# Kernel tuning notes

Measured on AMD Instinct MI355X. Metric: run time of the kernel, lower is better.

Reference implementation:

```python
import jax, jax.numpy as jnp
import numpy as np

B = 512      # streamlines (graphs in the batch)
L = 128      # points per streamline
M = L - 1    # edges per direction per streamline == conv output length
IN = 3       # 3-D coordinates
K = 5        # kNN neighbors (self included, as in PyG knn)
FOV = 5      # conv kernel; odd so conv out length == M, matching the batch vector
PAD = FOV // 2
NC = 2
EPS = 1e-5


def _bn(x, g, b, m, v):
    # inference-mode BatchNorm1d
    return (x - m) * jax.lax.rsqrt(v + EPS) * g + b


def setup_inputs():
    key = jax.random.key(0)
    ks = jax.random.split(key, 20)
    r = lambda i, shape: jax.random.normal(ks[i], shape, jnp.float32) * 0.05
    ones = lambda n: jnp.ones((n,), jnp.float32)
    zeros = lambda n: jnp.zeros((n,), jnp.float32)
    pos = jax.random.normal(ks[0], (B * L, IN), jnp.float32)
    # consecutive-point (forward) edges, streamline-major order
    base = (jnp.arange(B)[:, None] * L + jnp.arange(M)[None, :]).reshape(-1)
    fwd = jnp.stack([base, base + 1]).astype(jnp.int32)          # [2, B*M]
    eidx = jnp.concatenate([fwd, fwd], axis=1)                   # [2, 2*B*M]; first half overwritten in forward
    batch = jnp.repeat(jnp.arange(B, dtype=jnp.int32), L)        # per-point graph id
    lengths = jnp.full((B,), L, dtype=jnp.int32)
    return dict(
        pos=pos, eidx=eidx, batch=batch, lengths=lengths,
        conv1_w=r(1, (FOV, 2 * IN, 64)), conv1_b=r(2, (64,)),
        bn1_g=ones(64), bn1_b=zeros(64), bn1_m=r(3, (64,)), bn1_v=ones(64),
        edge_w=r(4, (2 * 64, 128)), edge_b=r(5, (128,)),
        bn2_g=ones(128), bn2_b=zeros(128), bn2_m=r(6, (128,)), bn2_v=ones(128),
        lin1_w=r(7, (64 + 128, 1024)), lin1_b=r(8, (1024,)),
        bn3_g=ones(1024), bn3_b=zeros(1024), bn3_m=r(9, (1024,)), bn3_v=ones(1024),
        m1_w=r(10, (1024, 512)), m1_b=r(11, (512,)),
        bn4_g=ones(512), bn4_b=zeros(512), bn4_m=r(12, (512,)), bn4_v=ones(512),
        m2_w=r(13, (512, 256)), m2_b=r(14, (256,)),
        bn5_g=ones(256), bn5_b=zeros(256), bn5_m=r(15, (256,)), bn5_v=ones(256),
        out_w=r(16, (256, NC)), out_b=r(17, (NC,)),
    )


def reference(pos, eidx, batch, lengths,
              conv1_w, conv1_b, bn1_g, bn1_b, bn1_m, bn1_v,
              edge_w, edge_b, bn2_g, bn2_b, bn2_m, bn2_v,
              lin1_w, lin1_b, bn3_g, bn3_b, bn3_m, bn3_v,
              m1_w, m1_b, bn4_g, bn4_b, bn4_m, bn4_v,
              m2_w, m2_b, bn5_g, bn5_b, bn5_m, bn5_v,
              out_w, out_b):
    E = eidx.shape[1]
    half = eidx[:, E // 2:]
    # eidx[:, :E//2] = eidx[:, E//2:].flip(1)
    eidx = jnp.concatenate([half[:, ::-1], half], axis=1)
    # irregular gather: edge features [E, 2*IN]
    feats = jnp.concatenate([pos[eidx[1]] - pos[eidx[0]], pos[eidx[0]]], axis=1)
    x = feats.reshape(2 * B, M, 2 * IN)                            # folded direction+batch
    # Conv1d (cross-correlation) -> BN -> ReLU, channels-last layout
    x = jax.lax.conv_general_dilated(x, conv1_w, (1,), [(PAD, PAD)],
                                     dimension_numbers=('NWC', 'WIO', 'NWC')) + conv1_b
    x = jax.nn.relu(_bn(x, bn1_g, bn1_b, bn1_m, bn1_v))            # [2B, M, 64]
    # direction symmetrization: max(first half, second half flipped on batch & length)
    x = jnp.maximum(x[:B], x[B:][::-1, ::-1, :])                   # [B, M, 64]
    x1 = x.reshape(B * M, 64)
    # ---- DynamicEdgeConv: per-streamline kNN graph + edge MLP + max aggregation ----
    xg = x1.reshape(B, M, 64)
    sq = jnp.sum(xg * xg, axis=-1)                                 # [B, M]
    dist = sq[:, :, None] + sq[:, None, :] - 2.0 * jnp.einsum('bmd,bnd->bmn', xg, xg)
    _, idx = jax.lax.top_k(-dist, K)                               # [B, M, K] (self included)
    xj = jax.vmap(lambda xs, ix: xs[ix])(xg, idx)                  # [B, M, K, 64]
    xi = jnp.broadcast_to(xg[:, :, None, :], xj.shape)
    ef = jnp.concatenate([xi, xj - xi], axis=-1)                   # [B, M, K, 128]
    ef = _bn(jax.nn.relu(ef @ edge_w + edge_b), bn2_g, bn2_b, bn2_m, bn2_v)
    x2 = jnp.max(ef, axis=2).reshape(B * M, 128)                   # max aggr over neighbors
    # ---- lin1 + global max pool + classifier MLP (dropout = identity in eval) ----
    h = jnp.concatenate([x1, x2], axis=1)                          # [N, 192]
    h = _bn(jax.nn.relu(h @ lin1_w + lin1_b), bn3_g, bn3_b, bn3_m, bn3_v)  # [N, 1024]
    g = jnp.max(h.reshape(B, M, 1024), axis=1)                     # global_max_pool -> [B, 1024]
    g = _bn(jax.nn.relu(g @ m1_w + m1_b), bn4_g, bn4_b, bn4_m, bn4_v)
    g = _bn(jax.nn.relu(g @ m2_w + m2_b), bn5_g, bn5_b, bn5_m, bn5_v)
    return g @ out_w + out_b                                       # [B, NC]
```

## Files before the change

kernel.cpp:

```cpp
#include <hip/hip_runtime.h>

#define BB 512
#define LL 128
#define MM 127
#define EPS 1e-5f

typedef _Float16 half4 __attribute__((ext_vector_type(4)));
typedef _Float16 half8 __attribute__((ext_vector_type(8)));
typedef float f32x16 __attribute__((ext_vector_type(16)));

#define HB_PITCH 384
#define HB_BATCH 49152

__global__ __launch_bounds__(256) void k0_prep(
    const float* __restrict__ lw, char* __restrict__ lwT,
    const float* __restrict__ ew, char* __restrict__ ewT,
    const float* __restrict__ m1w, char* __restrict__ m1wT,
    const float* __restrict__ m2w, char* __restrict__ m2wT)
{
  int tid = threadIdx.x;
  __shared__ float ws2[256][32];
  if (blockIdx.x < 32) {
    int c0 = blockIdx.x * 32;
    __shared__ float wcol[192][32];
    for (int i = tid; i < 192 * 32; i += 256) {
      int k = i >> 5, c = i & 31;
      wcol[k][c] = lw[k * 1024 + c0 + c];
    }
    __syncthreads();
    for (int j = tid; j < 768; j += 256) {
      int kg = j >> 5, c = j & 31;
      half8 v;
#pragma unroll
      for (int jj = 0; jj < 8; jj++) v[jj] = (_Float16)wcol[kg * 8 + jj][c];
      int cc = c0 + c;
      *(half8*)(lwT + cc * HB_PITCH + ((kg * 16) ^ ((cc & 7) << 4))) = v;
    }
  } else if (blockIdx.x == 32) {
    __shared__ float es[128][128];
    for (int i = tid; i < 128 * 128; i += 256) es[i >> 7][i & 127] = ew[i];
    __syncthreads();
    for (int i = tid; i < 256 * 8; i += 256) {
      int c = i >> 3, kg = i & 7;
      half8 v;
#pragma unroll
      for (int jj = 0; jj < 8; jj++) {
        int k = kg * 8 + jj;
        float val = (c < 128) ? (es[k][c] - es[64 + k][c]) : es[64 + k][c - 128];
        v[jj] = (_Float16)val;
      }
      *(half8*)(ewT + c * 128 + ((kg * 16) ^ ((c & 7) << 4))) = v;
    }
  } else {
    const float* src; char* dst; int N, K, c0, k0;
    if (blockIdx.x < 97) {
      int bb = blockIdx.x - 33;
      src = m1w; dst = m1wT; N = 512; K = 1024;
      c0 = (bb >> 2) * 32; k0 = (bb & 3) * 256;
    } else {
      int bb = blockIdx.x - 97;
      src = m2w; dst = m2wT; N = 256; K = 512;
      c0 = (bb >> 1) * 32; k0 = (bb & 1) * 256;
    }
    for (int i = tid; i < 256 * 32; i += 256) {
      int k = i >> 5, c = i & 31;
      ws2[k][c] = src[(size_t)(k0 + k) * N + c0 + c];
    }
    __syncthreads();
    for (int j = tid; j < 32 * 32; j += 256) {
      int kg = j >> 5, c = j & 31;
      half8 v;
#pragma unroll
      for (int jj = 0; jj < 8; jj++) v[jj] = (_Float16)ws2[kg * 8 + jj][c];
      int cc = c0 + c;
      *(half8*)(dst + (size_t)cc * (2 * K) + ((2 * (k0 + kg * 8)) ^ ((cc & 7) << 4))) = v;
    }
  }
}

__global__ __launch_bounds__(256) void k1a_conv(
    const float* __restrict__ pos, const float* __restrict__ cw,
    const float* __restrict__ cb, const float* __restrict__ g1,
    const float* __restrict__ b1, const float* __restrict__ m1,
    const float* __restrict__ v1, char* __restrict__ hb,
    float* __restrict__ xgr)
{
  int b = blockIdx.x;
  int tid = threadIdx.x;
  __shared__ float fpad[132][8];

  if (tid < 40) {
    int rr = tid >> 3;
    int row = (rr < 2) ? rr : (127 + rr);
    fpad[row][tid & 7] = 0.f;
  }
  const float* pb = pos + b * LL * 3;
  for (int i = tid; i < MM * 6; i += 256) {
    int m = i / 6, c = i % 6;
    float v = (c < 3) ? (pb[(m + 1) * 3 + c] - pb[m * 3 + c]) : pb[m * 3 + c - 3];
    fpad[m + 2][c] = v;
  }
  int orow = BB - 1 - b;
  char* hbb = hb + (size_t)orow * HB_BATCH;
  float* xgb = xgr + (size_t)orow * 8192;
  if (tid < 8) *(float4*)(hbb + 127 * HB_PITCH + tid * 16) = make_float4(0.f, 0.f, 0.f, 0.f);
  if (tid < 16) *(float4*)(xgb + 127 * 64 + tid * 4) = make_float4(0.f, 0.f, 0.f, 0.f);

  int c = tid & 63, cg = tid >> 6;
  float wreg[30];
#pragma unroll
  for (int t = 0; t < 5; t++)
#pragma unroll
    for (int ci = 0; ci < 6; ci++) wreg[t * 6 + ci] = cw[(t * 6 + ci) * 64 + c];
  float s1 = g1[c] * rsqrtf(v1[c] + EPS);
  float t1 = (cb[c] - m1[c]) * s1 + b1[c];
  __syncthreads();

#pragma unroll
  for (int it = 0; it < 8; it++) {
    int chunk = cg + 4 * it;
    int m0 = chunk * 4;
    float4 fa[8], fb[8];
#pragma unroll
    for (int r = 0; r < 8; r++) {
      fa[r] = *(const float4*)&fpad[m0 + r][0];
      fb[r] = *(const float4*)&fpad[m0 + r][4];
    }
#pragma unroll
    for (int mm = 0; mm < 4; mm++) {
      int m = m0 + mm;
      if (m >= MM) continue;
      float af = 0.f, ab = 0.f;
#pragma unroll
      for (int t = 0; t < 5; t++) {
#pragma unroll
        for (int ci = 0; ci < 6; ci++) {
          float w = wreg[t * 6 + ci];
          int rf = mm + t, rb = mm + 4 - t;
          float xf = (ci < 4) ? ((const float*)&fa[rf])[ci] : ((const float*)&fb[rf])[ci - 4];
          float xb = (ci < 4) ? ((const float*)&fa[rb])[ci] : ((const float*)&fb[rb])[ci - 4];
          af = fmaf(xf, w, af);
          ab = fmaf(xb, w, ab);
        }
      }
      float z = fmaxf(af, ab) * s1 + t1;
      float xv = fmaxf(z, 0.f);
      int p = MM - 1 - m;
      xgb[p * 64 + (((c >> 2) + (p >> 3)) & 15) * 4 + (c & 3)] = xv;
      *(_Float16*)(hbb + p * HB_PITCH + ((2 * c) ^ ((p & 7) << 4))) = (_Float16)xv;
    }
  }
}

__global__ __launch_bounds__(256, 2) void k1b_knn(
    const float* __restrict__ xgr, int* __restrict__ idxb)
{
  int bid = blockIdx.x;
  int ob = bid >> 1, hf = bid & 1;
  int r0 = hf * 64;
  int tid = threadIdx.x;
  __shared__ float xs[128][64];
  __shared__ float sq[128];
  __shared__ float S[64][132];
  __shared__ float bsl[4][64][5];
  __shared__ int   bil[4][64][5];

  const float4* src = (const float4*)(xgr + (size_t)ob * 8192);
  for (int i = tid; i < 2048; i += 256) ((float4*)xs)[i] = src[i];
  __syncthreads();
  if (tid < 128) {
    int r = tid;
    float s = 0.f;
#pragma unroll
    for (int c4 = 0; c4 < 16; c4++) {
      float4 v = *(const float4*)&xs[r][((c4 + (r >> 3)) & 15) * 4];
      s = fmaf(v.x, v.x, s); s = fmaf(v.y, v.y, s);
      s = fmaf(v.z, v.z, s); s = fmaf(v.w, v.w, s);
    }
    sq[r] = s;
  }
  __syncthreads();
  {
    int tr = tid >> 4, tc = tid & 15;
    int ra = r0 + tr * 4;
    int ga = ra >> 3;
    float acc[4][8];
#pragma unroll
    for (int i = 0; i < 4; i++)
#pragma unroll
      for (int j = 0; j < 8; j++) acc[i][j] = 0.f;
    for (int k4 = 0; k4 < 16; k4++) {
      int ca = ((k4 + ga) & 15) * 4;
      int cbo = ((k4 + tc) & 15) * 4;
      float4 av[4], bv[8];
#pragma unroll
      for (int i = 0; i < 4; i++) av[i] = *(const float4*)&xs[ra + i][ca];
#pragma unroll
      for (int j = 0; j < 8; j++) bv[j] = *(const float4*)&xs[tc * 8 + j][cbo];
#pragma unroll
      for (int i = 0; i < 4; i++)
#pragma unroll
        for (int j = 0; j < 8; j++) {
          acc[i][j] = fmaf(av[i].x, bv[j].x, acc[i][j]);
          acc[i][j] = fmaf(av[i].y, bv[j].y, acc[i][j]);
          acc[i][j] = fmaf(av[i].z, bv[j].z, acc[i][j]);
          acc[i][j] = fmaf(av[i].w, bv[j].w, acc[i][j]);
        }
    }
    float sqc[8];
#pragma unroll
    for (int j = 0; j < 8; j++) sqc[j] = sq[tc * 8 + j];
#pragma unroll
    for (int i = 0; i < 4; i++) {
      float4 s0, s1v;
      s0.x = sqc[0] - 2.f * acc[i][0]; s0.y = sqc[1] - 2.f * acc[i][1];
      s0.z = sqc[2] - 2.f * acc[i][2]; s0.w = sqc[3] - 2.f * acc[i][3];
      s1v.x = sqc[4] - 2.f * acc[i][4]; s1v.y = sqc[5] - 2.f * acc[i][5];
      s1v.z = sqc[6] - 2.f * acc[i][6]; s1v.w = sqc[7] - 2.f * acc[i][7];
      *(float4*)&S[tr * 4 + i][tc * 8]     = s0;
      *(float4*)&S[tr * 4 + i][tc * 8 + 4] = s1v;
    }
  }
  __syncthreads();
  {
    int row = tid & 63, q = tid >> 6;
    float bs[5]; int bi[5];
#pragma unroll
    for (int k = 0; k < 5; k++) { bs[k] = 1e30f; bi[k] = 0; }
#pragma unroll
    for (int e4 = 0; e4 < 8; e4++) {
      float4 sv = *(const float4*)&S[row][q * 32 + e4 * 4];
      int cbase = q * 32 + e4 * 4;
      float va[4] = {sv.x, sv.y, sv.z, sv.w};
#pragma unroll
      for (int e = 0; e < 4; e++) {
        int col = cbase + e;
        float sc = va[e];
        if (col < 127 && sc < bs[4]) {
          bs[4] = sc; bi[4] = col;
#pragma unroll
          for (int k = 3; k >= 0; k--) {
            if (bs[k + 1] < bs[k]) {
              float ts = bs[k]; bs[k] = bs[k + 1]; bs[k + 1] = ts;
              int ti = bi[k]; bi[k] = bi[k + 1]; bi[k + 1] = ti;
            }
          }
        }
      }
    }
#pragma unroll
    for (int k = 0; k < 5; k++) { bsl[q][row][k] = bs[k]; bil[q][row][k] = bi[k]; }
  }
  __syncthreads();
  if (tid < 64) {
    int i = r0 + tid;
    if (i < MM) {
      int i0 = 0, i1 = 0, i2 = 0, i3 = 0;
      int base = (ob * MM + i) * 5;
#pragma unroll
      for (int k = 0; k < 5; k++) {
        float v0 = bsl[0][tid][i0], v1 = bsl[1][tid][i1];
        float v2 = bsl[2][tid][i2], v3 = bsl[3][tid][i3];
        float best = v0; int q = 0;
        if (v1 < best) { best = v1; q = 1; }
        if (v2 < best) { best = v2; q = 2; }
        if (v3 < best) { best = v3; q = 3; }
        int iq = (q == 0) ? i0 : (q == 1) ? i1 : (q == 2) ? i2 : i3;
        idxb[base + k] = bil[q][tid][iq];
        if (q == 0) i0++; else if (q == 1) i1++; else if (q == 2) i2++; else i3++;
      }
    }
  }
}

__global__ __launch_bounds__(256) void k3_edge(
    const int* __restrict__ idxb, const char* __restrict__ ewT,
    const float* __restrict__ eb, const float* __restrict__ g2,
    const float* __restrict__ b2, const float* __restrict__ m2,
    const float* __restrict__ v2, char* __restrict__ hb)
{
  int b = blockIdx.x;
  int tid = threadIdx.x;
  int w = tid >> 6, l = tid & 63;
  int lo = l & 31, hi = l >> 5;
  __shared__ _Float16 vvs[MM][136];
  __shared__ int idxs[MM * 5];
  char* hbb = hb + (size_t)b * HB_BATCH;

  for (int i = tid; i < MM * 5; i += 256) idxs[i] = idxb[b * MM * 5 + i];
  if (tid < 16) *(float4*)(hbb + 127 * HB_PITCH + 128 + tid * 16) = make_float4(0.f, 0.f, 0.f, 0.f);

  half8 af[4][4];
#pragma unroll
  for (int rt = 0; rt < 4; rt++) {
    int row = rt * 32 + lo;
    const char* rb = hbb + row * HB_PITCH;
    int sz = (row & 7) << 4;
#pragma unroll
    for (int ks = 0; ks < 4; ks++)
      af[rt][ks] = *(const half8*)(rb + ((ks * 32 + hi * 16) ^ sz));
  }
  int cu = w * 32 + lo;
  int swzW = (cu & 7) << 4;
  const char* wu = ewT + cu * 128;
  const char* wv = ewT + (128 + cu) * 128;
  half8 bu[4], bv[4];
#pragma unroll
  for (int ks = 0; ks < 4; ks++) {
    int off = (ks * 32 + hi * 16) ^ swzW;
    bu[ks] = *(const half8*)(wu + off);
    bv[ks] = *(const half8*)(wv + off);
  }
  f32x16 accu[4], accv[4];
#pragma unroll
  for (int rt = 0; rt < 4; rt++)
#pragma unroll
    for (int r = 0; r < 16; r++) { accu[rt][r] = 0.f; accv[rt][r] = 0.f; }
#pragma unroll
  for (int ks = 0; ks < 4; ks++)
#pragma unroll
    for (int rt = 0; rt < 4; rt++) {
      accu[rt] = __builtin_amdgcn_mfma_f32_32x32x16_f16(af[rt][ks], bu[ks], accu[rt], 0, 0, 0);
      accv[rt] = __builtin_amdgcn_mfma_f32_32x32x16_f16(af[rt][ks], bv[ks], accv[rt], 0, 0, 0);
    }
#pragma unroll
  for (int rt = 0; rt < 4; rt++)
#pragma unroll
    for (int r = 0; r < 16; r++) {
      int p = rt * 32 + (r & 3) + 8 * (r >> 2) + 4 * hi;
      if (p < MM) vvs[p][cu] = (_Float16)accv[rt][r];
    }
  __syncthreads();
  float ebv = eb[cu];
  float s2 = g2[cu] * rsqrtf(v2[cu] + EPS);
  float t2 = b2[cu] - m2[cu] * s2;
#pragma unroll
  for (int rt = 0; rt < 4; rt++)
#pragma unroll
    for (int r = 0; r < 16; r++) {
      int p = rt * 32 + (r & 3) + 8 * (r >> 2) + 4 * hi;
      if (p >= MM) continue;
      const int* ip = &idxs[p * 5];
      float u = accu[rt][r];
      float mx = -1e30f;
#pragma unroll
      for (int k = 0; k < 5; k++)
        mx = fmaxf(mx, u + (float)vvs[ip[k]][cu]);
      float o = fmaxf(mx + ebv, 0.f) * s2 + t2;
      *(_Float16*)(hbb + p * HB_PITCH + ((128 + 2 * cu) ^ ((p & 7) << 4))) = (_Float16)o;
    }
}

__global__ __launch_bounds__(512, 2) void k4_lin1(
    const char* __restrict__ hb, const char* __restrict__ lwT,
    const float* __restrict__ lb, const float* __restrict__ g3,
    const float* __restrict__ b3, const float* __restrict__ m3,
    const float* __restrict__ v3, char* __restrict__ gbufh)
{
  int b = blockIdx.x;
  int tid = threadIdx.x;
  int w = tid >> 6;
  int rh = w >> 2, cq = w & 3;
  int l = tid & 63;
  int lo = l & 31, hi = l >> 5;
  __shared__ __align__(16) char sA[HB_BATCH];
  __shared__ float rmslab[2][1024];

  {
    const char* gA = hb + (size_t)b * HB_BATCH;
#pragma unroll
    for (int i = 0; i < 6; i++)
      *(float4*)(sA + (i * 512 + tid) * 16) = *(const float4*)(gA + (i * 512 + tid) * 16);
  }
  __syncthreads();

  int sz = (lo & 7) << 4;
  half8 af[2][12];
#pragma unroll
  for (int q = 0; q < 2; q++) {
    const char* rbase = sA + ((rh * 2 + q) * 32 + lo) * HB_PITCH;
#pragma unroll
    for (int ks = 0; ks < 12; ks++)
      af[q][ks] = *(const half8*)(rbase + ((ks * 32 + hi * 16) ^ sz));
  }

  int col0 = cq * 256 + lo;
  half8 bf[2][12];
  {
    const char* cb0 = lwT + (size_t)col0 * HB_PITCH;
#pragma unroll
    for (int ks = 0; ks < 12; ks++)
      bf[0][ks] = *(const half8*)(cb0 + ((ks * 32 + hi * 16) ^ sz));
  }
#pragma unroll
  for (int ct = 0; ct < 8; ct++) {
    if (ct < 7) {
      const char* cbn = lwT + (size_t)(col0 + (ct + 1) * 32) * HB_PITCH;
#pragma unroll
      for (int ks = 0; ks < 12; ks++)
        bf[(ct + 1) & 1][ks] = *(const half8*)(cbn + ((ks * 32 + hi * 16) ^ sz));
    }
    f32x16 acc[2];
#pragma unroll
    for (int q = 0; q < 2; q++)
#pragma unroll
      for (int r = 0; r < 16; r++) acc[q][r] = 0.f;
#pragma unroll
    for (int ks = 0; ks < 12; ks++) {
      acc[0] = __builtin_amdgcn_mfma_f32_32x32x16_f16(af[0][ks], bf[ct & 1][ks], acc[0], 0, 0, 0);
      acc[1] = __builtin_amdgcn_mfma_f32_32x32x16_f16(af[1][ks], bf[ct & 1][ks], acc[1], 0, 0, 0);
    }
    int col = col0 + ct * 32;
    float bias = lb[col];
    float rm = 0.f;
#pragma unroll
    for (int q = 0; q < 2; q++)
#pragma unroll
      for (int r = 0; r < 16; r++) {
        float v = fmaxf(acc[q][r] + bias, 0.f);
        if (q == 1 && r == 15) v = (rh == 1 && hi == 1) ? 0.f : v;
        rm = fmaxf(rm, v);
      }
    rm = fmaxf(rm, __shfl_xor(rm, 32));
    if (hi == 0) rmslab[rh][col] = rm;
  }
  __syncthreads();
  if (tid < 256) {
    half4 o;
#pragma unroll
    for (int j = 0; j < 4; j++) {
      int c = tid * 4 + j;
      float mv = fmaxf(rmslab[0][c], rmslab[1][c]);
      float s = g3[c] * rsqrtf(v3[c] + EPS);
      float t = b3[c] - m3[c] * s;
      o[j] = (_Float16)(mv * s + t);
    }
    *(half4*)(gbufh + (size_t)b * 2048 + ((8 * tid) ^ ((b & 7) << 4))) = o;
  }
}

template<int K, int N>
__global__ __launch_bounds__(64) void k5_gemm(
    const char* __restrict__ inh, const char* __restrict__ wT,
    const float* __restrict__ bias, const float* __restrict__ gg,
    const float* __restrict__ bbp, const float* __restrict__ mmp,
    const float* __restrict__ vvp, char* __restrict__ outh,
    float* __restrict__ outf)
{
  constexpr int NT = N / 32;
  constexpr int NC = K / 128;
  int bid = blockIdx.x;
  int mt = bid / NT, nt = bid % NT;
  int l = threadIdx.x;
  int lo = l & 31, hi = l >> 5;
  int row = mt * 32 + lo, col = nt * 32 + lo;
  const char* arow = inh + (size_t)row * (2 * K);
  const char* brow = wT + (size_t)col * (2 * K);
  int sza = (row & 7) << 4, szb = (col & 7) << 4;

  half8 a[2][8], bf[2][8];
#pragma unroll
  for (int ks = 0; ks < 8; ks++) {
    int off = ks * 32 + hi * 16;
    a[0][ks]  = *(const half8*)(arow + (off ^ sza));
    bf[0][ks] = *(const half8*)(brow + (off ^ szb));
  }
  f32x16 acc;
#pragma unroll
  for (int r = 0; r < 16; r++) acc[r] = 0.f;
#pragma unroll
  for (int c = 0; c < NC; c++) {
    if (c + 1 < NC) {
#pragma unroll
      for (int ks = 0; ks < 8; ks++) {
        int off = (c + 1) * 256 + ks * 32 + hi * 16;
        a[(c + 1) & 1][ks]  = *(const half8*)(arow + (off ^ sza));
        bf[(c + 1) & 1][ks] = *(const half8*)(brow + (off ^ szb));
      }
    }
#pragma unroll
    for (int ks = 0; ks < 8; ks++)
      acc = __builtin_amdgcn_mfma_f32_32x32x16_f16(a[c & 1][ks], bf[c & 1][ks], acc, 0, 0, 0);
  }
  float bv = bias[col];
  float s = gg[col] * rsqrtf(vvp[col] + EPS);
  float t = bbp[col] - mmp[col] * s;
#pragma unroll
  for (int r = 0; r < 16; r++) {
    float z = fmaxf(acc[r] + bv, 0.f) * s + t;
    int orow = mt * 32 + (r & 3) + 8 * (r >> 2) + 4 * hi;
    if (outh)
      *(_Float16*)(outh + (size_t)orow * (2 * N) + ((2 * col) ^ ((orow & 7) << 4))) = (_Float16)z;
    else
      outf[(size_t)orow * N + col] = z;
  }
}

__global__ __launch_bounds__(256) void k5c_out(
    const float* __restrict__ c2, const float* __restrict__ ow,
    const float* __restrict__ ob, float* __restrict__ out)
{
  int t = blockIdx.x * 256 + threadIdx.x;
  int r = t >> 1, c = t & 1;
  float acc = 0.f;
  for (int d4 = 0; d4 < 64; d4++) {
    float4 cv = *(const float4*)(c2 + r * 256 + d4 * 4);
    acc = fmaf(cv.x, ow[(d4 * 4 + 0) * 2 + c], acc);
    acc = fmaf(cv.y, ow[(d4 * 4 + 1) * 2 + c], acc);
    acc = fmaf(cv.z, ow[(d4 * 4 + 2) * 2 + c], acc);
    acc = fmaf(cv.w, ow[(d4 * 4 + 3) * 2 + c], acc);
  }
  out[t] = acc + ob[c];
}

extern "C" void kernel_launch(void* const* d_in, const int* in_sizes, int n_in,
                              void* d_out, int out_size, void* d_ws, size_t ws_size,
                              hipStream_t stream)
{
  const float* pos = (const float*)d_in[0];
  const float* cw  = (const float*)d_in[4];
  const float* cb  = (const float*)d_in[5];
  const float* g1  = (const float*)d_in[6];
  const float* b1  = (const float*)d_in[7];
  const float* m1  = (const float*)d_in[8];
  const float* v1  = (const float*)d_in[9];
  const float* ew  = (const float*)d_in[10];
  const float* eb  = (const float*)d_in[11];
  const float* g2  = (const float*)d_in[12];
  const float* b2  = (const float*)d_in[13];
  const float* m2  = (const float*)d_in[14];
  const float* v2  = (const float*)d_in[15];
  const float* lw  = (const float*)d_in[16];
  const float* lb  = (const float*)d_in[17];
  const float* g3  = (const float*)d_in[18];
  const float* b3  = (const float*)d_in[19];
  const float* m3  = (const float*)d_in[20];
  const float* v3  = (const float*)d_in[21];
  const float* m1w = (const float*)d_in[22];
  const float* m1b = (const float*)d_in[23];
  const float* g4  = (const float*)d_in[24];
  const float* b4  = (const float*)d_in[25];
  const float* m4  = (const float*)d_in[26];
  const float* v4  = (const float*)d_in[27];
  const float* m2w = (const float*)d_in[28];
  const float* m2b = (const float*)d_in[29];
  const float* g5  = (const float*)d_in[30];
  const float* b5  = (const float*)d_in[31];
  const float* m5  = (const float*)d_in[32];
  const float* v5  = (const float*)d_in[33];
  const float* ow  = (const float*)d_in[34];
  const float* ob  = (const float*)d_in[35];

  char* ws = (char*)d_ws;
  char*  hb    = ws;
  char*  lwT   = ws + 25165824;
  char*  ewT   = ws + 25559040;
  int*   idxb  = (int*)(ws + 25591808);
  char*  gbufh = ws + 26892288;
  char*  m1wT  = ws + 27940864;
  char*  c1h   = ws + 28989440;
  char*  m2wT  = ws + 29513728;
  float* c2    = (float*)(ws + 29775872);
  float* xgr   = (float*)(ws + 30300160);

  hipLaunchKernelGGL(k0_prep, dim3(113), dim3(256), 0, stream,
                     lw, lwT, ew, ewT, m1w, m1wT, m2w, m2wT);
  hipLaunchKernelGGL(k1a_conv, dim3(512), dim3(256), 0, stream,
                     pos, cw, cb, g1, b1, m1, v1, hb, xgr);
  hipLaunchKernelGGL(k1b_knn, dim3(1024), dim3(256), 0, stream, xgr, idxb);
  hipLaunchKernelGGL(k3_edge, dim3(512), dim3(256), 0, stream,
                     idxb, ewT, eb, g2, b2, m2, v2, hb);
  hipLaunchKernelGGL(k4_lin1, dim3(512), dim3(512), 0, stream,
                     hb, lwT, lb, g3, b3, m3, v3, gbufh);
  (k5_gemm<1024, 512>)<<<dim3(256), dim3(64), 0, stream>>>(
      gbufh, m1wT, m1b, g4, b4, m4, v4, c1h, nullptr);
  (k5_gemm<512, 256>)<<<dim3(128), dim3(64), 0, stream>>>(
      c1h, m2wT, m2b, g5, b5, m5, v5, nullptr, c2);
  hipLaunchKernelGGL(k5c_out, dim3(4), dim3(256), 0, stream,
                     c2, ow, ob, (float*)d_out);
}
```

Before: 127.2 us.

## Fuse classifier head GEMMs into one kernel and restructure kNN per streamline

```diff
diff --git a/kernel.cpp b/kernel.cpp
--- a/kernel.cpp
+++ b/kernel.cpp
@@ -155,15 +155,12 @@
 __global__ __launch_bounds__(256, 2) void k1b_knn(
     const float* __restrict__ xgr, int* __restrict__ idxb)
 {
-  int bid = blockIdx.x;
-  int ob = bid >> 1, hf = bid & 1;
-  int r0 = hf * 64;
+  int ob = blockIdx.x;
   int tid = threadIdx.x;
   __shared__ float xs[128][64];
   __shared__ float sq[128];
-  __shared__ float S[64][132];
-  __shared__ float bsl[4][64][5];
-  __shared__ int   bil[4][64][5];
+  __shared__ float bsl[8][128][5];
+  __shared__ int   bil[8][128][5];
 
   const float4* src = (const float4*)(xgr + (size_t)ob * 8192);
   for (int i = tid; i < 2048; i += 256) ((float4*)xs)[i] = src[i];
@@ -180,95 +177,85 @@
     sq[r] = s;
   }
   __syncthreads();
-  {
-    int tr = tid >> 4, tc = tid & 15;
-    int ra = r0 + tr * 4;
-    int ga = ra >> 3;
-    float acc[4][8];
+
+  int tr = tid & 31, cs = tid >> 5;
+  int ra = tr * 4;
+  int ga = ra >> 3;
+  float acc[4][16];
+#pragma unroll
+  for (int i = 0; i < 4; i++)
+#pragma unroll
+    for (int j = 0; j < 16; j++) acc[i][j] = 0.f;
+  for (int k4 = 0; k4 < 16; k4++) {
+    int ca = ((k4 + ga) & 15) * 4;
+    float4 av[4], bv[16];
+#pragma unroll
+    for (int i = 0; i < 4; i++) av[i] = *(const float4*)&xs[ra + i][ca];
+#pragma unroll
+    for (int jj = 0; jj < 16; jj++) {
+      int gb = cs * 2 + (jj >> 3);
+      bv[jj] = *(const float4*)&xs[cs * 16 + jj][((k4 + gb) & 15) * 4];
+    }
 #pragma unroll
     for (int i = 0; i < 4; i++)
 #pragma unroll
-      for (int j = 0; j < 8; j++) acc[i][j] = 0.f;
-    for (int k4 = 0; k4 < 16; k4++) {
-      int ca = ((k4 + ga) & 15) * 4;
-      int cbo = ((k4 + tc) & 15) * 4;
-      float4 av[4], bv[8];
-#pragma unroll
-      for (int i = 0; i < 4; i++) av[i] = *(const float4*)&xs[ra + i][ca];
-#pragma unroll
-      for (int j = 0; j < 8; j++) bv[j] = *(const float4*)&xs[tc * 8 + j][cbo];
-#pragma unroll
-      for (int i = 0; i < 4; i++)
-#pragma unroll
-        for (int j = 0; j < 8; j++) {
-          acc[i][j] = fmaf(av[i].x, bv[j].x, acc[i][j]);
-          acc[i][j] = fmaf(av[i].y, bv[j].y, acc[i][j]);
-          acc[i][j] = fmaf(av[i].z, bv[j].z, acc[i][j]);
-          acc[i][j] = fmaf(av[i].w, bv[j].w, acc[i][j]);
-        }
-    }
-    float sqc[8];
-#pragma unroll
-    for (int j = 0; j < 8; j++) sqc[j] = sq[tc * 8 + j];
-#pragma unroll
-    for (int i = 0; i < 4; i++) {
-      float4 s0, s1v;
-      s0.x = sqc[0] - 2.f * acc[i][0]; s0.y = sqc[1] - 2.f * acc[i][1];
-      s0.z = sqc[2] - 2.f * acc[i][2]; s0.w = sqc[3] - 2.f * acc[i][3];
-      s1v.x = sqc[4] - 2.f * acc[i][4]; s1v.y = sqc[5] - 2.f * acc[i][5];
-      s1v.z = sqc[6] - 2.f * acc[i][6]; s1v.w = sqc[7] - 2.f * acc[i][7];
-      *(float4*)&S[tr * 4 + i][tc * 8]     = s0;
-      *(float4*)&S[tr * 4 + i][tc * 8 + 4] = s1v;
-    }
-  }
-  __syncthreads();
-  {
-    int row = tid & 63, q = tid >> 6;
+      for (int jj = 0; jj < 16; jj++) {
+        acc[i][jj] = fmaf(av[i].x, bv[jj].x, acc[i][jj]);
+        acc[i][jj] = fmaf(av[i].y, bv[jj].y, acc[i][jj]);
+        acc[i][jj] = fmaf(av[i].z, bv[jj].z, acc[i][jj]);
+        acc[i][jj] = fmaf(av[i].w, bv[jj].w, acc[i][jj]);
+      }
+  }
+  float sqv[16];
+#pragma unroll
+  for (int jj = 0; jj < 16; jj++) sqv[jj] = sq[cs * 16 + jj];
+#pragma unroll
+  for (int i = 0; i < 4; i++) {
     float bs[5]; int bi[5];
 #pragma unroll
     for (int k = 0; k < 5; k++) { bs[k] = 1e30f; bi[k] = 0; }
 #pragma unroll
-    for (int e4 = 0; e4 < 8; e4++) {
-      float4 sv = *(const float4*)&S[row][q * 32 + e4 * 4];
-      int cbase = q * 32 + e4 * 4;
-      float va[4] = {sv.x, sv.y, sv.z, sv.w};
-#pragma unroll
-      for (int e = 0; e < 4; e++) {
-        int col = cbase + e;
-        float sc = va[e];
-        if (col < 127 && sc < bs[4]) {
-          bs[4] = sc; bi[4] = col;
-#pragma unroll
-          for (int k = 3; k >= 0; k--) {
-            if (bs[k + 1] < bs[k]) {
-              float ts = bs[k]; bs[k] = bs[k + 1]; bs[k + 1] = ts;
-              int ti = bi[k]; bi[k] = bi[k + 1]; bi[k + 1] = ti;
-            }
+    for (int jj = 0; jj < 16; jj++) {
+      int col = cs * 16 + jj;
+      float sc = sqv[jj] - 2.f * acc[i][jj];
+      if (col < 127 && sc < bs[4]) {
+        bs[4] = sc; bi[4] = col;
+#pragma unroll
+        for (int k = 3; k >= 0; k--) {
+          if (bs[k + 1] < bs[k]) {
+            float ts = bs[k]; bs[k] = bs[k + 1]; bs[k + 1] = ts;
+            int ti = bi[k]; bi[k] = bi[k + 1]; bi[k + 1] = ti;
           }
         }
       }
     }
 #pragma unroll
-    for (int k = 0; k < 5; k++) { bsl[q][row][k] = bs[k]; bil[q][row][k] = bi[k]; }
-  }
-  __syncthreads();
-  if (tid < 64) {
-    int i = r0 + tid;
-    if (i < MM) {
-      int i0 = 0, i1 = 0, i2 = 0, i3 = 0;
-      int base = (ob * MM + i) * 5;
-#pragma unroll
-      for (int k = 0; k < 5; k++) {
-        float v0 = bsl[0][tid][i0], v1 = bsl[1][tid][i1];
-        float v2 = bsl[2][tid][i2], v3 = bsl[3][tid][i3];
-        float best = v0; int q = 0;
-        if (v1 < best) { best = v1; q = 1; }
-        if (v2 < best) { best = v2; q = 2; }
-        if (v3 < best) { best = v3; q = 3; }
-        int iq = (q == 0) ? i0 : (q == 1) ? i1 : (q == 2) ? i2 : i3;
-        idxb[base + k] = bil[q][tid][iq];
-        if (q == 0) i0++; else if (q == 1) i1++; else if (q == 2) i2++; else i3++;
-      }
+    for (int k = 0; k < 5; k++) { bsl[cs][ra + i][k] = bs[k]; bil[cs][ra + i][k] = bi[k]; }
+  }
+  __syncthreads();
+  if (tid < MM) {
+    int i0 = 0, i1 = 0, i2 = 0, i3 = 0, i4 = 0, i5 = 0, i6 = 0, i7 = 0;
+    int base = (ob * MM + tid) * 5;
+#pragma unroll
+    for (int k = 0; k < 5; k++) {
+      float v0 = bsl[0][tid][i0], v1 = bsl[1][tid][i1];
+      float v2 = bsl[2][tid][i2], v3 = bsl[3][tid][i3];
+      float v4 = bsl[4][tid][i4], v5 = bsl[5][tid][i5];
+      float v6 = bsl[6][tid][i6], v7 = bsl[7][tid][i7];
+      float best = v0; int q = 0;
+      if (v1 < best) { best = v1; q = 1; }
+      if (v2 < best) { best = v2; q = 2; }
+      if (v3 < best) { best = v3; q = 3; }
+      if (v4 < best) { best = v4; q = 4; }
+      if (v5 < best) { best = v5; q = 5; }
+      if (v6 < best) { best = v6; q = 6; }
+      if (v7 < best) { best = v7; q = 7; }
+      int iq = (q == 0) ? i0 : (q == 1) ? i1 : (q == 2) ? i2 : (q == 3) ? i3 :
+               (q == 4) ? i4 : (q == 5) ? i5 : (q == 6) ? i6 : i7;
+      idxb[base + k] = bil[q][tid][iq];
+      if (q == 0) i0++; else if (q == 1) i1++; else if (q == 2) i2++;
+      else if (q == 3) i3++; else if (q == 4) i4++; else if (q == 5) i5++;
+      else if (q == 6) i6++; else i7++;
     }
   }
 }
@@ -439,78 +426,96 @@
   }
 }
 
-template<int K, int N>
-__global__ __launch_bounds__(64) void k5_gemm(
-    const char* __restrict__ inh, const char* __restrict__ wT,
-    const float* __restrict__ bias, const float* __restrict__ gg,
-    const float* __restrict__ bbp, const float* __restrict__ mmp,
-    const float* __restrict__ vvp, char* __restrict__ outh,
-    float* __restrict__ outf)
-{
-  constexpr int NT = N / 32;
-  constexpr int NC = K / 128;
-  int bid = blockIdx.x;
-  int mt = bid / NT, nt = bid % NT;
-  int l = threadIdx.x;
+__global__ __launch_bounds__(256) void k5_head(
+    const char* __restrict__ gbufh, const char* __restrict__ m1wT,
+    const float* __restrict__ m1b, const float* __restrict__ g4,
+    const float* __restrict__ b4, const float* __restrict__ m4,
+    const float* __restrict__ v4, const char* __restrict__ m2wT,
+    const float* __restrict__ m2b, const float* __restrict__ g5,
+    const float* __restrict__ b5, const float* __restrict__ m5,
+    const float* __restrict__ v5, const float* __restrict__ ow,
+    const float* __restrict__ ob, float* __restrict__ out)
+{
+  int mt = blockIdx.x;
+  int tid = threadIdx.x;
+  int w = tid >> 6, l = tid & 63;
   int lo = l & 31, hi = l >> 5;
-  int row = mt * 32 + lo, col = nt * 32 + lo;
-  const char* arow = inh + (size_t)row * (2 * K);
-  const char* brow = wT + (size_t)col * (2 * K);
-  int sza = (row & 7) << 4, szb = (col & 7) << 4;
-
-  half8 a[2][8], bf[2][8];
-#pragma unroll
-  for (int ks = 0; ks < 8; ks++) {
-    int off = ks * 32 + hi * 16;
-    a[0][ks]  = *(const half8*)(arow + (off ^ sza));
-    bf[0][ks] = *(const half8*)(brow + (off ^ szb));
-  }
-  f32x16 acc;
-#pragma unroll
-  for (int r = 0; r < 16; r++) acc[r] = 0.f;
-#pragma unroll
-  for (int c = 0; c < NC; c++) {
-    if (c + 1 < NC) {
-#pragma unroll
-      for (int ks = 0; ks < 8; ks++) {
-        int off = (c + 1) * 256 + ks * 32 + hi * 16;
-        a[(c + 1) & 1][ks]  = *(const half8*)(arow + (off ^ sza));
-        bf[(c + 1) & 1][ks] = *(const half8*)(brow + (off ^ szb));
-      }
-    }
-#pragma unroll
-    for (int ks = 0; ks < 8; ks++)
-      acc = __builtin_amdgcn_mfma_f32_32x32x16_f16(a[c & 1][ks], bf[c & 1][ks], acc, 0, 0, 0);
-  }
-  float bv = bias[col];
-  float s = gg[col] * rsqrtf(vvp[col] + EPS);
-  float t = bbp[col] - mmp[col] * s;
-#pragma unroll
-  for (int r = 0; r < 16; r++) {
-    float z = fmaxf(acc[r] + bv, 0.f) * s + t;
-    int orow = mt * 32 + (r & 3) + 8 * (r >> 2) + 4 * hi;
-    if (outh)
-      *(_Float16*)(outh + (size_t)orow * (2 * N) + ((2 * col) ^ ((orow & 7) << 4))) = (_Float16)z;
-    else
-      outf[(size_t)orow * N + col] = z;
-  }
-}
-
-__global__ __launch_bounds__(256) void k5c_out(
-    const float* __restrict__ c2, const float* __restrict__ ow,
-    const float* __restrict__ ob, float* __restrict__ out)
-{
-  int t = blockIdx.x * 256 + threadIdx.x;
-  int r = t >> 1, c = t & 1;
-  float acc = 0.f;
-  for (int d4 = 0; d4 < 64; d4++) {
-    float4 cv = *(const float4*)(c2 + r * 256 + d4 * 4);
-    acc = fmaf(cv.x, ow[(d4 * 4 + 0) * 2 + c], acc);
-    acc = fmaf(cv.y, ow[(d4 * 4 + 1) * 2 + c], acc);
-    acc = fmaf(cv.z, ow[(d4 * 4 + 2) * 2 + c], acc);
-    acc = fmaf(cv.w, ow[(d4 * 4 + 3) * 2 + c], acc);
-  }
-  out[t] = acc + ob[c];
+  __shared__ __align__(16) char c1s[32 * 1024];
+  __shared__ float c2s[32][268];
+
+  int row = mt * 32 + lo;
+  const char* arow = gbufh + (size_t)row * 2048;
+  int sza = (row & 7) << 4;
+
+#pragma unroll
+  for (int ct = 0; ct < 4; ct++) {
+    int col = w * 128 + ct * 32 + lo;
+    const char* brow = m1wT + (size_t)col * 2048;
+    int szb = (col & 7) << 4;
+    f32x16 acc;
+#pragma unroll
+    for (int r = 0; r < 16; r++) acc[r] = 0.f;
+#pragma unroll
+    for (int ks = 0; ks < 64; ks++) {
+      int off = ks * 32 + hi * 16;
+      half8 a  = *(const half8*)(arow + (off ^ sza));
+      half8 bf = *(const half8*)(brow + (off ^ szb));
+      acc = __builtin_amdgcn_mfma_f32_32x32x16_f16(a, bf, acc, 0, 0, 0);
+    }
+    float bv = m1b[col];
+    float s = g4[col] * rsqrtf(v4[col] + EPS);
+    float t = b4[col] - m4[col] * s;
+#pragma unroll
+    for (int r = 0; r < 16; r++) {
+      float z = fmaxf(acc[r] + bv, 0.f) * s + t;
+      int orw = (r & 3) + 8 * (r >> 2) + 4 * hi;
+      *(_Float16*)(c1s + orw * 1024 + ((2 * col) ^ ((orw & 7) << 4))) = (_Float16)z;
+    }
+  }
+  __syncthreads();
+
+  const char* arow2 = c1s + lo * 1024;
+  int sza2 = (lo & 7) << 4;
+#pragma unroll
+  for (int ct = 0; ct < 2; ct++) {
+    int col = w * 64 + ct * 32 + lo;
+    const char* brow = m2wT + (size_t)col * 1024;
+    int szb = (col & 7) << 4;
+    f32x16 acc;
+#pragma unroll
+    for (int r = 0; r < 16; r++) acc[r] = 0.f;
+#pragma unroll
+    for (int ks = 0; ks < 32; ks++) {
+      int off = ks * 32 + hi * 16;
+      half8 a  = *(const half8*)(arow2 + (off ^ sza2));
+      half8 bf = *(const half8*)(brow + (off ^ szb));
+      acc = __builtin_amdgcn_mfma_f32_32x32x16_f16(a, bf, acc, 0, 0, 0);
+    }
+    float bv = m2b[col];
+    float s = g5[col] * rsqrtf(v5[col] + EPS);
+    float t = b5[col] - m5[col] * s;
+#pragma unroll
+    for (int r = 0; r < 16; r++) {
+      float z = fmaxf(acc[r] + bv, 0.f) * s + t;
+      int orw = (r & 3) + 8 * (r >> 2) + 4 * hi;
+      c2s[orw][col] = z;
+    }
+  }
+  __syncthreads();
+
+  if (tid < 64) {
+    int r = tid >> 1, c = tid & 1;
+    float acc = 0.f;
+#pragma unroll
+    for (int d4 = 0; d4 < 64; d4++) {
+      float4 cv = *(const float4*)&c2s[r][d4 * 4];
+      acc = fmaf(cv.x, ow[(d4 * 4 + 0) * 2 + c], acc);
+      acc = fmaf(cv.y, ow[(d4 * 4 + 1) * 2 + c], acc);
+      acc = fmaf(cv.z, ow[(d4 * 4 + 2) * 2 + c], acc);
+      acc = fmaf(cv.w, ow[(d4 * 4 + 3) * 2 + c], acc);
+    }
+    out[(mt * 32 + r) * 2 + c] = acc + ob[c];
+  }
 }
 
 extern "C" void kernel_launch(void* const* d_in, const int* in_sizes, int n_in,
@@ -558,24 +563,19 @@
   int*   idxb  = (int*)(ws + 25591808);
   char*  gbufh = ws + 26892288;
   char*  m1wT  = ws + 27940864;
-  char*  c1h   = ws + 28989440;
-  char*  m2wT  = ws + 29513728;
-  float* c2    = (float*)(ws + 29775872);
-  float* xgr   = (float*)(ws + 30300160);
+  char*  m2wT  = ws + 28989440;
+  float* xgr   = (float*)(ws + 29251584);
 
   hipLaunchKernelGGL(k0_prep, dim3(113), dim3(256), 0, stream,
                      lw, lwT, ew, ewT, m1w, m1wT, m2w, m2wT);
   hipLaunchKernelGGL(k1a_conv, dim3(512), dim3(256), 0, stream,
                      pos, cw, cb, g1, b1, m1, v1, hb, xgr);
-  hipLaunchKernelGGL(k1b_knn, dim3(1024), dim3(256), 0, stream, xgr, idxb);
+  hipLaunchKernelGGL(k1b_knn, dim3(512), dim3(256), 0, stream, xgr, idxb);
   hipLaunchKernelGGL(k3_edge, dim3(512), dim3(256), 0, stream,
                      idxb, ewT, eb, g2, b2, m2, v2, hb);
   hipLaunchKernelGGL(k4_lin1, dim3(512), dim3(512), 0, stream,
                      hb, lwT, lb, g3, b3, m3, v3, gbufh);
-  (k5_gemm<1024, 512>)<<<dim3(256), dim3(64), 0, stream>>>(
-      gbufh, m1wT, m1b, g4, b4, m4, v4, c1h, nullptr);
-  (k5_gemm<512, 256>)<<<dim3(128), dim3(64), 0, stream>>>(
-      c1h, m2wT, m2b, g5, b5, m5, v5, nullptr, c2);
-  hipLaunchKernelGGL(k5c_out, dim3(4), dim3(256), 0, stream,
-                     c2, ow, ob, (float*)d_out);
-}
+  hipLaunchKernelGGL(k5_head, dim3(16), dim3(256), 0, stream,
+                     gbufh, m1wT, m1b, g4, b4, m4, v4,
+                     m2wT, m2b, g5, b5, m5, v5, ow, ob, (float*)d_out);
+}
```

Result: slower. 222.3 us (+74.9%).

## Fuse kNN distance tiles with per-thread top-k, one block per streamline

Applied to the files above, without the earlier changes.

```diff
diff --git a/kernel.cpp b/kernel.cpp
--- a/kernel.cpp
+++ b/kernel.cpp
@@ -155,15 +155,12 @@
 __global__ __launch_bounds__(256, 2) void k1b_knn(
     const float* __restrict__ xgr, int* __restrict__ idxb)
 {
-  int bid = blockIdx.x;
-  int ob = bid >> 1, hf = bid & 1;
-  int r0 = hf * 64;
+  int ob = blockIdx.x;
   int tid = threadIdx.x;
   __shared__ float xs[128][64];
   __shared__ float sq[128];
-  __shared__ float S[64][132];
-  __shared__ float bsl[4][64][5];
-  __shared__ int   bil[4][64][5];
+  __shared__ float bsl[8][128][5];
+  __shared__ int   bil[8][128][5];
 
   const float4* src = (const float4*)(xgr + (size_t)ob * 8192);
   for (int i = tid; i < 2048; i += 256) ((float4*)xs)[i] = src[i];
@@ -180,95 +177,85 @@
     sq[r] = s;
   }
   __syncthreads();
-  {
-    int tr = tid >> 4, tc = tid & 15;
-    int ra = r0 + tr * 4;
-    int ga = ra >> 3;
-    float acc[4][8];
+
+  int tr = tid & 31, cs = tid >> 5;
+  int ra = tr * 4;
+  int ga = ra >> 3;
+  float acc[4][16];
+#pragma unroll
+  for (int i = 0; i < 4; i++)
+#pragma unroll
+    for (int j = 0; j < 16; j++) acc[i][j] = 0.f;
+  for (int k4 = 0; k4 < 16; k4++) {
+    int ca = ((k4 + ga) & 15) * 4;
+    float4 av[4], bv[16];
+#pragma unroll
+    for (int i = 0; i < 4; i++) av[i] = *(const float4*)&xs[ra + i][ca];
+#pragma unroll
+    for (int jj = 0; jj < 16; jj++) {
+      int gb = cs * 2 + (jj >> 3);
+      bv[jj] = *(const float4*)&xs[cs * 16 + jj][((k4 + gb) & 15) * 4];
+    }
 #pragma unroll
     for (int i = 0; i < 4; i++)
 #pragma unroll
-      for (int j = 0; j < 8; j++) acc[i][j] = 0.f;
-    for (int k4 = 0; k4 < 16; k4++) {
-      int ca = ((k4 + ga) & 15) * 4;
-      int cbo = ((k4 + tc) & 15) * 4;
-      float4 av[4], bv[8];
-#pragma unroll
-      for (int i = 0; i < 4; i++) av[i] = *(const float4*)&xs[ra + i][ca];
-#pragma unroll
-      for (int j = 0; j < 8; j++) bv[j] = *(const float4*)&xs[tc * 8 + j][cbo];
-#pragma unroll
-      for (int i = 0; i < 4; i++)
-#pragma unroll
-        for (int j = 0; j < 8; j++) {
-          acc[i][j] = fmaf(av[i].x, bv[j].x, acc[i][j]);
-          acc[i][j] = fmaf(av[i].y, bv[j].y, acc[i][j]);
-          acc[i][j] = fmaf(av[i].z, bv[j].z, acc[i][j]);
-          acc[i][j] = fmaf(av[i].w, bv[j].w, acc[i][j]);
-        }
-    }
-    float sqc[8];
-#pragma unroll
-    for (int j = 0; j < 8; j++) sqc[j] = sq[tc * 8 + j];
-#pragma unroll
-    for (int i = 0; i < 4; i++) {
-      float4 s0, s1v;
-      s0.x = sqc[0] - 2.f * acc[i][0]; s0.y = sqc[1] - 2.f * acc[i][1];
-      s0.z = sqc[2] - 2.f * acc[i][2]; s0.w = sqc[3] - 2.f * acc[i][3];
-      s1v.x = sqc[4] - 2.f * acc[i][4]; s1v.y = sqc[5] - 2.f * acc[i][5];
-      s1v.z = sqc[6] - 2.f * acc[i][6]; s1v.w = sqc[7] - 2.f * acc[i][7];
-      *(float4*)&S[tr * 4 + i][tc * 8]     = s0;
-      *(float4*)&S[tr * 4 + i][tc * 8 + 4] = s1v;
-    }
-  }
-  __syncthreads();
-  {
-    int row = tid & 63, q = tid >> 6;
+      for (int jj = 0; jj < 16; jj++) {
+        acc[i][jj] = fmaf(av[i].x, bv[jj].x, acc[i][jj]);
+        acc[i][jj] = fmaf(av[i].y, bv[jj].y, acc[i][jj]);
+        acc[i][jj] = fmaf(av[i].z, bv[jj].z, acc[i][jj]);
+        acc[i][jj] = fmaf(av[i].w, bv[jj].w, acc[i][jj]);
+      }
+  }
+  float sqv[16];
+#pragma unroll
+  for (int jj = 0; jj < 16; jj++) sqv[jj] = sq[cs * 16 + jj];
+#pragma unroll
+  for (int i = 0; i < 4; i++) {
     float bs[5]; int bi[5];
 #pragma unroll
     for (int k = 0; k < 5; k++) { bs[k] = 1e30f; bi[k] = 0; }
 #pragma unroll
-    for (int e4 = 0; e4 < 8; e4++) {
-      float4 sv = *(const float4*)&S[row][q * 32 + e4 * 4];
-      int cbase = q * 32 + e4 * 4;
-      float va[4] = {sv.x, sv.y, sv.z, sv.w};
-#pragma unroll
-      for (int e = 0; e < 4; e++) {
-        int col = cbase + e;
-        float sc = va[e];
-        if (col < 127 && sc < bs[4]) {
-          bs[4] = sc; bi[4] = col;
-#pragma unroll
-          for (int k = 3; k >= 0; k--) {
-            if (bs[k + 1] < bs[k]) {
-              float ts = bs[k]; bs[k] = bs[k + 1]; bs[k + 1] = ts;
-              int ti = bi[k]; bi[k] = bi[k + 1]; bi[k + 1] = ti;
-            }
+    for (int jj = 0; jj < 16; jj++) {
+      int col = cs * 16 + jj;
+      float sc = sqv[jj] - 2.f * acc[i][jj];
+      if (col < 127 && sc < bs[4]) {
+        bs[4] = sc; bi[4] = col;
+#pragma unroll
+        for (int k = 3; k >= 0; k--) {
+          if (bs[k + 1] < bs[k]) {
+            float ts = bs[k]; bs[k] = bs[k + 1]; bs[k + 1] = ts;
+            int ti = bi[k]; bi[k] = bi[k + 1]; bi[k + 1] = ti;
           }
         }
       }
     }
 #pragma unroll
-    for (int k = 0; k < 5; k++) { bsl[q][row][k] = bs[k]; bil[q][row][k] = bi[k]; }
-  }
-  __syncthreads();
-  if (tid < 64) {
-    int i = r0 + tid;
-    if (i < MM) {
-      int i0 = 0, i1 = 0, i2 = 0, i3 = 0;
-      int base = (ob * MM + i) * 5;
-#pragma unroll
-      for (int k = 0; k < 5; k++) {
-        float v0 = bsl[0][tid][i0], v1 = bsl[1][tid][i1];
-        float v2 = bsl[2][tid][i2], v3 = bsl[3][tid][i3];
-        float best = v0; int q = 0;
-        if (v1 < best) { best = v1; q = 1; }
-        if (v2 < best) { best = v2; q = 2; }
-        if (v3 < best) { best = v3; q = 3; }
-        int iq = (q == 0) ? i0 : (q == 1) ? i1 : (q == 2) ? i2 : i3;
-        idxb[base + k] = bil[q][tid][iq];
-        if (q == 0) i0++; else if (q == 1) i1++; else if (q == 2) i2++; else i3++;
-      }
+    for (int k = 0; k < 5; k++) { bsl[cs][ra + i][k] = bs[k]; bil[cs][ra + i][k] = bi[k]; }
+  }
+  __syncthreads();
+  if (tid < MM) {
+    int i0 = 0, i1 = 0, i2 = 0, i3 = 0, i4 = 0, i5 = 0, i6 = 0, i7 = 0;
+    int base = (ob * MM + tid) * 5;
+#pragma unroll
+    for (int k = 0; k < 5; k++) {
+      float v0 = bsl[0][tid][i0], v1 = bsl[1][tid][i1];
+      float v2 = bsl[2][tid][i2], v3 = bsl[3][tid][i3];
+      float v4 = bsl[4][tid][i4], v5 = bsl[5][tid][i5];
+      float v6 = bsl[6][tid][i6], v7 = bsl[7][tid][i7];
+      float best = v0; int q = 0;
+      if (v1 < best) { best = v1; q = 1; }
+      if (v2 < best) { best = v2; q = 2; }
+      if (v3 < best) { best = v3; q = 3; }
+      if (v4 < best) { best = v4; q = 4; }
+      if (v5 < best) { best = v5; q = 5; }
+      if (v6 < best) { best = v6; q = 6; }
+      if (v7 < best) { best = v7; q = 7; }
+      int iq = (q == 0) ? i0 : (q == 1) ? i1 : (q == 2) ? i2 : (q == 3) ? i3 :
+               (q == 4) ? i4 : (q == 5) ? i5 : (q == 6) ? i6 : i7;
+      idxb[base + k] = bil[q][tid][iq];
+      if (q == 0) i0++; else if (q == 1) i1++; else if (q == 2) i2++;
+      else if (q == 3) i3++; else if (q == 4) i4++; else if (q == 5) i5++;
+      else if (q == 6) i6++; else i7++;
     }
   }
 }
@@ -567,7 +554,7 @@
                      lw, lwT, ew, ewT, m1w, m1wT, m2w, m2wT);
   hipLaunchKernelGGL(k1a_conv, dim3(512), dim3(256), 0, stream,
                      pos, cw, cb, g1, b1, m1, v1, hb, xgr);
-  hipLaunchKernelGGL(k1b_knn, dim3(1024), dim3(256), 0, stream, xgr, idxb);
+  hipLaunchKernelGGL(k1b_knn, dim3(512), dim3(256), 0, stream, xgr, idxb);
   hipLaunchKernelGGL(k3_edge, dim3(512), dim3(256), 0, stream,
                      idxb, ewT, eb, g2, b2, m2, v2, hb);
   hipLaunchKernelGGL(k4_lin1, dim3(512), dim3(512), 0, stream,
```

Result: slower. 148.9 us (+17.1%).

## Split kNN distance tile into two column passes to cut LDS and raise occupancy

Applied to the files above, without the earlier changes.

```diff
diff --git a/kernel.cpp b/kernel.cpp
--- a/kernel.cpp
+++ b/kernel.cpp
@@ -152,7 +152,7 @@
   }
 }
 
-__global__ __launch_bounds__(256, 2) void k1b_knn(
+__global__ __launch_bounds__(256, 3) void k1b_knn(
     const float* __restrict__ xgr, int* __restrict__ idxb)
 {
   int bid = blockIdx.x;
@@ -161,9 +161,7 @@
   int tid = threadIdx.x;
   __shared__ float xs[128][64];
   __shared__ float sq[128];
-  __shared__ float S[64][132];
-  __shared__ float bsl[4][64][5];
-  __shared__ int   bil[4][64][5];
+  __shared__ float S[64][68];
 
   const float4* src = (const float4*)(xgr + (size_t)ob * 8192);
   for (int i = tid; i < 2048; i += 256) ((float4*)xs)[i] = src[i];
@@ -180,95 +178,88 @@
     sq[r] = s;
   }
   __syncthreads();
-  {
-    int tr = tid >> 4, tc = tid & 15;
-    int ra = r0 + tr * 4;
-    int ga = ra >> 3;
-    float acc[4][8];
-#pragma unroll
-    for (int i = 0; i < 4; i++)
-#pragma unroll
-      for (int j = 0; j < 8; j++) acc[i][j] = 0.f;
-    for (int k4 = 0; k4 < 16; k4++) {
-      int ca = ((k4 + ga) & 15) * 4;
-      int cbo = ((k4 + tc) & 15) * 4;
-      float4 av[4], bv[8];
-#pragma unroll
-      for (int i = 0; i < 4; i++) av[i] = *(const float4*)&xs[ra + i][ca];
-#pragma unroll
-      for (int j = 0; j < 8; j++) bv[j] = *(const float4*)&xs[tc * 8 + j][cbo];
+
+  int tr = tid >> 4, tc = tid & 15;
+  int ra = r0 + tr * 4;
+  int ga = ra >> 3;
+  float bs[5]; int bi[5];
+#pragma unroll
+  for (int k = 0; k < 5; k++) { bs[k] = 1e30f; bi[k] = 0; }
+
+#pragma unroll
+  for (int pass = 0; pass < 2; pass++) {
+    {
+      int j0 = pass * 64 + tc * 4;
+      int gb = pass * 8 + (tc >> 1);
+      float acc[4][4];
 #pragma unroll
       for (int i = 0; i < 4; i++)
 #pragma unroll
-        for (int j = 0; j < 8; j++) {
-          acc[i][j] = fmaf(av[i].x, bv[j].x, acc[i][j]);
-          acc[i][j] = fmaf(av[i].y, bv[j].y, acc[i][j]);
-          acc[i][j] = fmaf(av[i].z, bv[j].z, acc[i][j]);
-          acc[i][j] = fmaf(av[i].w, bv[j].w, acc[i][j]);
-        }
-    }
-    float sqc[8];
-#pragma unroll
-    for (int j = 0; j < 8; j++) sqc[j] = sq[tc * 8 + j];
-#pragma unroll
-    for (int i = 0; i < 4; i++) {
-      float4 s0, s1v;
-      s0.x = sqc[0] - 2.f * acc[i][0]; s0.y = sqc[1] - 2.f * acc[i][1];
-      s0.z = sqc[2] - 2.f * acc[i][2]; s0.w = sqc[3] - 2.f * acc[i][3];
-      s1v.x = sqc[4] - 2.f * acc[i][4]; s1v.y = sqc[5] - 2.f * acc[i][5];
-      s1v.z = sqc[6] - 2.f * acc[i][6]; s1v.w = sqc[7] - 2.f * acc[i][7];
-      *(float4*)&S[tr * 4 + i][tc * 8]     = s0;
-      *(float4*)&S[tr * 4 + i][tc * 8 + 4] = s1v;
-    }
-  }
-  __syncthreads();
-  {
-    int row = tid & 63, q = tid >> 6;
-    float bs[5]; int bi[5];
-#pragma unroll
-    for (int k = 0; k < 5; k++) { bs[k] = 1e30f; bi[k] = 0; }
-#pragma unroll
-    for (int e4 = 0; e4 < 8; e4++) {
-      float4 sv = *(const float4*)&S[row][q * 32 + e4 * 4];
-      int cbase = q * 32 + e4 * 4;
-      float va[4] = {sv.x, sv.y, sv.z, sv.w};
-#pragma unroll
-      for (int e = 0; e < 4; e++) {
-        int col = cbase + e;
-        float sc = va[e];
-        if (col < 127 && sc < bs[4]) {
-          bs[4] = sc; bi[4] = col;
-#pragma unroll
-          for (int k = 3; k >= 0; k--) {
-            if (bs[k + 1] < bs[k]) {
-              float ts = bs[k]; bs[k] = bs[k + 1]; bs[k + 1] = ts;
-              int ti = bi[k]; bi[k] = bi[k + 1]; bi[k + 1] = ti;
+        for (int j = 0; j < 4; j++) acc[i][j] = 0.f;
+      for (int k4 = 0; k4 < 16; k4++) {
+        int ca = ((k4 + ga) & 15) * 4;
+        int cbo = ((k4 + gb) & 15) * 4;
+        float4 av[4], bv[4];
+#pragma unroll
+        for (int i = 0; i < 4; i++) av[i] = *(const float4*)&xs[ra + i][ca];
+#pragma unroll
+        for (int j = 0; j < 4; j++) bv[j] = *(const float4*)&xs[j0 + j][cbo];
+#pragma unroll
+        for (int i = 0; i < 4; i++)
+#pragma unroll
+          for (int j = 0; j < 4; j++) {
+            acc[i][j] = fmaf(av[i].x, bv[j].x, acc[i][j]);
+            acc[i][j] = fmaf(av[i].y, bv[j].y, acc[i][j]);
+            acc[i][j] = fmaf(av[i].z, bv[j].z, acc[i][j]);
+            acc[i][j] = fmaf(av[i].w, bv[j].w, acc[i][j]);
+          }
+      }
+      float sqc[4];
+#pragma unroll
+      for (int j = 0; j < 4; j++) sqc[j] = sq[j0 + j];
+#pragma unroll
+      for (int i = 0; i < 4; i++) {
+        float4 s0;
+        s0.x = sqc[0] - 2.f * acc[i][0];
+        s0.y = sqc[1] - 2.f * acc[i][1];
+        s0.z = sqc[2] - 2.f * acc[i][2];
+        s0.w = sqc[3] - 2.f * acc[i][3];
+        *(float4*)&S[tr * 4 + i][tc * 4] = s0;
+      }
+    }
+    __syncthreads();
+    if (tid < 64) {
+      int row = tid;
+#pragma unroll
+      for (int e4 = 0; e4 < 16; e4++) {
+        float4 sv = *(const float4*)&S[row][e4 * 4];
+        int cbase = pass * 64 + e4 * 4;
+        float va[4] = {sv.x, sv.y, sv.z, sv.w};
+#pragma unroll
+        for (int e = 0; e < 4; e++) {
+          int col = cbase + e;
+          float sc = va[e];
+          if (col < 127 && sc < bs[4]) {
+            bs[4] = sc; bi[4] = col;
+#pragma unroll
+            for (int k = 3; k >= 0; k--) {
+              if (bs[k + 1] < bs[k]) {
+                float ts = bs[k]; bs[k] = bs[k + 1]; bs[k + 1] = ts;
+                int ti = bi[k]; bi[k] = bi[k + 1]; bi[k + 1] = ti;
+              }
             }
           }
         }
       }
     }
-#pragma unroll
-    for (int k = 0; k < 5; k++) { bsl[q][row][k] = bs[k]; bil[q][row][k] = bi[k]; }
-  }
-  __syncthreads();
+    __syncthreads();
+  }
   if (tid < 64) {
     int i = r0 + tid;
     if (i < MM) {
-      int i0 = 0, i1 = 0, i2 = 0, i3 = 0;
       int base = (ob * MM + i) * 5;
 #pragma unroll
-      for (int k = 0; k < 5; k++) {
-        float v0 = bsl[0][tid][i0], v1 = bsl[1][tid][i1];
-        float v2 = bsl[2][tid][i2], v3 = bsl[3][tid][i3];
-        float best = v0; int q = 0;
-        if (v1 < best) { best = v1; q = 1; }
-        if (v2 < best) { best = v2; q = 2; }
-        if (v3 < best) { best = v3; q = 3; }
-        int iq = (q == 0) ? i0 : (q == 1) ? i1 : (q == 2) ? i2 : i3;
-        idxb[base + k] = bil[q][tid][iq];
-        if (q == 0) i0++; else if (q == 1) i1++; else if (q == 2) i2++; else i3++;
-      }
+      for (int k = 0; k < 5; k++) idxb[base + k] = bi[k];
     }
   }
 }
```

Result: slower. 209.3 us (+64.6%).
